# Performance work log

Measured on AMD Instinct MI355X. Metric: run time of the kernel, lower is better.

The kernel has to match this reference:

```python
import jax, jax.numpy as jnp
import numpy as np


def setup_inputs() -> dict:
    key = jax.random.key(0)
    ks = jax.random.split(key, 10)
    B, S, C, H, NC, T = 128, 512, 512, 512, 64, 25
    s = 0.02  # init scale
    return {
        "x": jax.random.normal(ks[0], (B, S, C), jnp.float32),
        "text": jax.random.randint(ks[1], (B, T + 1), 0, NC),
        "W_i2h": jax.random.normal(ks[2], (C, H), jnp.float32) * s,
        "W_h2h": jax.random.normal(ks[3], (H, H), jnp.float32) * s,
        "b_h2h": jnp.zeros((H,), jnp.float32),
        "W_score": jax.random.normal(ks[4], (H, 1), jnp.float32) * s,
        "W_lstm": jax.random.normal(ks[5], (C + NC, 4 * H), jnp.float32) * s,
        "U_lstm": jax.random.normal(ks[6], (H, 4 * H), jnp.float32) * s,
        "b_lstm": jnp.zeros((4 * H,), jnp.float32),
        "W_gen": jax.random.normal(ks[7], (H, NC), jnp.float32) * s,
        "b_gen": jnp.zeros((NC,), jnp.float32),
        "batch_max_length": 25,
    }


def reference(x, text, W_i2h, W_h2h, b_h2h, W_score, W_lstm, U_lstm, b_lstm,
              W_gen, b_gen, batch_max_length):
    B = x.shape[0]
    H = W_h2h.shape[0]
    NC = W_gen.shape[1]
    T = batch_max_length

    # i2h(batch_H) is loop-invariant -> compute once. [B,S,H]
    batch_H_proj = jnp.einsum('bsc,ch->bsh', x, W_i2h)
    # one-hot teacher-forcing inputs, time-major for scan. [T,B,NC]
    onehots_t = jnp.swapaxes(jax.nn.one_hot(text[:, :T], NC, dtype=x.dtype), 0, 1)

    def step(carry, char_oh):
        h, c = carry
        hp = (h @ W_h2h + b_h2h)[:, None, :]                 # [B,1,H]
        e = jnp.tanh(batch_H_proj + hp) @ W_score            # [B,S,1]
        alpha = jax.nn.softmax(e, axis=1)                    # [B,S,1]
        context = jnp.einsum('bs,bsc->bc', alpha[..., 0], x) # [B,C]
        inp = jnp.concatenate([context, char_oh], axis=1)    # [B,C+NC]
        # Keras LSTMCell gate math: z split into i,f,g,o chunks
        z = inp @ W_lstm + h @ U_lstm + b_lstm               # [B,4H]
        zi, zf, zg, zo = jnp.split(z, 4, axis=1)
        i = jax.nn.sigmoid(zi)
        f = jax.nn.sigmoid(zf)
        g = jnp.tanh(zg)
        o = jax.nn.sigmoid(zo)
        c_new = f * c + i * g
        h_new = o * jnp.tanh(c_new)
        return (h_new, c_new), h_new

    init = (jnp.zeros((B, H), x.dtype), jnp.zeros((B, H), x.dtype))
    _, hs = jax.lax.scan(step, init, onehots_t)              # [T,B,H]
    output_hiddens = jnp.swapaxes(hs, 0, 1)                  # [B,T,H]
    probs = output_hiddens @ W_gen + b_gen                   # [B,T,NC]
    return probs
```

## Files before the change

### kernel.cpp

```cpp
#include <hip/hip_runtime.h>
#include <hip/hip_bf16.h>

#define B_ 128
#define S_ 512
#define C_ 512
#define H_ 512
#define NC_ 64
#define T_ 25
#define TEXTW (T_ + 1)

typedef __attribute__((ext_vector_type(8))) short bf16x8;
typedef __attribute__((ext_vector_type(8))) unsigned short u16x8;
typedef __attribute__((ext_vector_type(4))) float f32x4;

__device__ __forceinline__ float bf2f(unsigned short u) {
    union { unsigned int i; float f; } v; v.i = ((unsigned int)u) << 16; return v.f;
}
__device__ __forceinline__ unsigned short f2bf(float f) {
    union { float f; unsigned int u; } v; v.f = f;
    unsigned int r = (v.u + 0x7FFFu + ((v.u >> 16) & 1u)) >> 16;
    return (unsigned short)r;
}
__device__ __forceinline__ void gload_lds16(const void* g, void* l) {
    __builtin_amdgcn_global_load_lds(
        (const __attribute__((address_space(1))) unsigned int*)g,
        (__attribute__((address_space(3))) unsigned int*)l, 16, 0, 0);
}
__device__ __forceinline__ float fast_tanh(float x) {
    float e = __builtin_amdgcn_exp2f(2.885390082f * x);
    return 1.f - 2.f * __builtin_amdgcn_rcpf(e + 1.f);
}
__device__ __forceinline__ float fast_sigmoid(float x) {
    return __builtin_amdgcn_rcpf(1.f + __builtin_amdgcn_exp2f(-1.442695041f * x));
}

__global__ __launch_bounds__(512) void setup_k(
    const float* __restrict__ Wi, const float* __restrict__ Wh,
    const float* __restrict__ Wl, const float* __restrict__ Ul,
    const float* __restrict__ bh,
    unsigned short* __restrict__ Wt_bf, unsigned short* __restrict__ Wh_bf,
    unsigned short* __restrict__ WU_t,
    float* __restrict__ c, float* __restrict__ hp, unsigned short* __restrict__ inp) {
    int blk = blockIdx.x, tid = threadIdx.x;
    if (blk < 128) {
        c[blk * 512 + tid] = 0.f;
        hp[blk * 512 + tid] = bh[tid];
        inp[blk * 1024 + 512 + tid] = 0;
    } else if (blk < 640) {
        int n = blk - 128;
        Wt_bf[n * 512 + tid] = f2bf(Wi[tid * 512 + n]);
    } else if (blk < 1152) {
        int i = (blk - 640) * 512 + tid;
        Wh_bf[i] = f2bf(Wh[i]);
    } else {
        int np = blk - 1152;
        int h = np >> 2, g = np & 3;
        {
            float v = Wl[(size_t)tid * 2048 + g * 512 + h];
            WU_t[(size_t)np * 1024 + tid] = f2bf(v);
        }
        {
            float v = Ul[(size_t)tid * 2048 + g * 512 + h];
            WU_t[(size_t)np * 1024 + 512 + tid] = f2bf(v);
        }
    }
}

__global__ __launch_bounds__(256) void conv_x(const float* __restrict__ in,
                                              unsigned short* __restrict__ out) {
    int i = blockIdx.x * 256 + threadIdx.x;
    const float4 v = ((const float4*)in)[i];
    ushort4 o;
    o.x = f2bf(v.x); o.y = f2bf(v.y); o.z = f2bf(v.z); o.w = f2bf(v.w);
    ((ushort4*)out)[i] = o;
}

__global__ __launch_bounds__(256) void gemm_proj(const unsigned short* __restrict__ A,
                                                 const unsigned short* __restrict__ Bt,
                                                 unsigned short* __restrict__ Cm) {
    __shared__ unsigned short As[128 * 64];
    __shared__ unsigned short Bs[128 * 64];
    int tid = threadIdx.x;
    int lane = tid & 63;
    int wid = tid >> 6;
    int wr = wid >> 1, wc = wid & 1;
    int row0 = blockIdx.y * 128;
    int col0 = blockIdx.x * 128;

    f32x4 acc[4][4];
#pragma unroll
    for (int i = 0; i < 4; ++i)
#pragma unroll
        for (int j = 0; j < 4; ++j) acc[i][j] = (f32x4){0.f, 0.f, 0.f, 0.f};

    for (int k0 = 0; k0 < 512; k0 += 64) {
#pragma unroll
        for (int i = 0; i < 4; ++i) {
            int e = tid + i * 256;
            int r = e >> 3, cc = e & 7;
            int cs = cc ^ (r & 7);
            gload_lds16(A + (size_t)(row0 + r) * 512 + k0 + cs * 8, &As[e * 8]);
        }
#pragma unroll
        for (int i = 0; i < 4; ++i) {
            int e = tid + i * 256;
            int r = e >> 3, cc = e & 7;
            int cs = cc ^ (r & 7);
            gload_lds16(Bt + (size_t)(col0 + r) * 512 + k0 + cs * 8, &Bs[e * 8]);
        }
        __syncthreads();
#pragma unroll
        for (int ks = 0; ks < 2; ++ks) {
            bf16x8 a[4], b[4];
#pragma unroll
            for (int i = 0; i < 4; ++i) {
                int m = wr * 64 + i * 16 + (lane & 15);
                int ch = (ks * 4 + (lane >> 4)) ^ (m & 7);
                a[i] = *(const bf16x8*)&As[(m * 8 + ch) * 8];
            }
#pragma unroll
            for (int j = 0; j < 4; ++j) {
                int n = wc * 64 + j * 16 + (lane & 15);
                int ch = (ks * 4 + (lane >> 4)) ^ (n & 7);
                b[j] = *(const bf16x8*)&Bs[(n * 8 + ch) * 8];
            }
#pragma unroll
            for (int i = 0; i < 4; ++i)
#pragma unroll
                for (int j = 0; j < 4; ++j)
                    acc[i][j] = __builtin_amdgcn_mfma_f32_16x16x32_bf16(a[i], b[j], acc[i][j], 0, 0, 0);
        }
        __syncthreads();
    }
#pragma unroll
    for (int i = 0; i < 4; ++i)
#pragma unroll
        for (int j = 0; j < 4; ++j) {
            int gcol = col0 + wc * 64 + j * 16 + (lane & 15);
#pragma unroll
            for (int r = 0; r < 4; ++r) {
                int grow = row0 + wr * 64 + i * 16 + (lane >> 4) * 4 + r;
                Cm[(size_t)grow * 512 + gcol] = f2bf(acc[i][j][r]);
            }
        }
}

__global__ __launch_bounds__(1024) void ectx_kernel(
    const unsigned short* __restrict__ proj, const unsigned short* __restrict__ xb,
    const float* __restrict__ hp, const float* __restrict__ Wscore,
    unsigned short* __restrict__ inp) {
    __shared__ float sh_e[512];
    __shared__ float sh_alpha[512];
    __shared__ float sh_red[16];
    __shared__ float shp[8][512];
    int b = blockIdx.x;
    int tid = threadIdx.x, wave = tid >> 6, lane = tid & 63;

    {
        float4 h0 = *(const float4*)(hp + b * 512 + lane * 8);
        float4 h1 = *(const float4*)(hp + b * 512 + lane * 8 + 4);
        float4 w0 = *(const float4*)(Wscore + lane * 8);
        float4 w1 = *(const float4*)(Wscore + lane * 8 + 4);
        float hp_r[8] = {h0.x, h0.y, h0.z, h0.w, h1.x, h1.y, h1.z, h1.w};
        float w_r[8]  = {w0.x, w0.y, w0.z, w0.w, w1.x, w1.y, w1.z, w1.w};
        float w2_r[8];
#pragma unroll
        for (int j = 0; j < 8; ++j) w2_r[j] = -2.f * w_r[j];
        int s0 = wave * 32;
        for (int i = 0; i < 32; i += 4) {
            bf16x8 pv[4];
#pragma unroll
            for (int q = 0; q < 4; ++q)
                pv[q] = *(const bf16x8*)(proj + ((size_t)(b * 512 + s0 + i + q) << 9) + lane * 8);
#pragma unroll
            for (int q = 0; q < 4; ++q) {
                float a = 0.f;
#pragma unroll
                for (int j = 0; j < 8; ++j) {
                    float xv = bf2f((unsigned short)pv[q][j]) + hp_r[j];
                    float r = __builtin_amdgcn_rcpf(__builtin_amdgcn_exp2f(2.885390082f * xv) + 1.f);
                    a += w_r[j];
                    a = fmaf(w2_r[j], r, a);
                }
#pragma unroll
                for (int off = 32; off > 0; off >>= 1) a += __shfl_xor(a, off, 64);
                if (lane == 0) sh_e[s0 + i + q] = a;
            }
        }
    }
    __syncthreads();

    if (tid < 512) {
        float v = sh_e[tid];
        float m = v;
#pragma unroll
        for (int off = 32; off > 0; off >>= 1) m = fmaxf(m, __shfl_xor(m, off, 64));
        if (lane == 0) sh_red[wave] = m;
    }
    __syncthreads();
    if (tid < 512) {
        float v = sh_e[tid];
        float mm = sh_red[0];
#pragma unroll
        for (int i = 1; i < 8; ++i) mm = fmaxf(mm, sh_red[i]);
        float p = __builtin_amdgcn_exp2f(1.442695041f * (v - mm));
        float ss = p;
#pragma unroll
        for (int off = 32; off > 0; off >>= 1) ss += __shfl_xor(ss, off, 64);
        if (lane == 0) sh_red[8 + wave] = ss;
        sh_alpha[tid] = p;
    }
    __syncthreads();
    {
        float tot = 0.f;
#pragma unroll
        for (int i = 0; i < 8; ++i) tot += sh_red[8 + i];
        float inv = __builtin_amdgcn_rcpf(tot);
        inv = inv * (2.f - tot * inv);
        if (tid < 512) sh_alpha[tid] = sh_alpha[tid] * inv;
    }
    __syncthreads();

    {
        int cc = wave >> 3, sg = wave & 7;
        int col = cc * 256 + lane * 4;
        float a0 = 0.f, a1 = 0.f, a2 = 0.f, a3 = 0.f;
#pragma unroll 4
        for (int s = sg; s < 512; s += 8) {
            float al = sh_alpha[s];
            ushort4 xv = *(const ushort4*)(xb + ((size_t)(b * 512 + s) << 9) + col);
            a0 = fmaf(al, bf2f(xv.x), a0);
            a1 = fmaf(al, bf2f(xv.y), a1);
            a2 = fmaf(al, bf2f(xv.z), a2);
            a3 = fmaf(al, bf2f(xv.w), a3);
        }
        *(float4*)&shp[sg][col] = make_float4(a0, a1, a2, a3);
    }
    __syncthreads();
    if (tid < 512) {
        float s = 0.f;
#pragma unroll
        for (int r = 0; r < 8; ++r) s += shp[r][tid];
        inp[b * 1024 + tid] = f2bf(s);
    }
}

__global__ __launch_bounds__(512) void z_gemm(const unsigned short* __restrict__ A,
                                              const unsigned short* __restrict__ Bt,
                                              float* __restrict__ Z) {
    __shared__ unsigned short As[8192];
    __shared__ unsigned short Bs[4096];
    int tid = threadIdx.x;
    int lane = tid & 63;
    int wave = tid >> 6;
    int wr = wave >> 2, wc = wave & 3;
    int col0 = blockIdx.x * 64;

    f32x4 acc[4];
#pragma unroll
    for (int i = 0; i < 4; ++i) acc[i] = (f32x4){0.f, 0.f, 0.f, 0.f};

    for (int k0 = 0; k0 < 1024; k0 += 64) {
#pragma unroll
        for (int i = 0; i < 2; ++i) {
            int e = tid + i * 512;
            int r = e >> 3, cc = e & 7;
            int cs = cc ^ (r & 7);
            gload_lds16(A + (size_t)r * 1024 + k0 + cs * 8, &As[e * 8]);
        }
        {
            int e = tid;
            int r = e >> 3, cc = e & 7;
            int cs = cc ^ (r & 7);
            gload_lds16(Bt + (size_t)(col0 + r) * 1024 + k0 + cs * 8, &Bs[e * 8]);
        }
        __syncthreads();
#pragma unroll
        for (int ks = 0; ks < 2; ++ks) {
            bf16x8 a[4], bfr;
#pragma unroll
            for (int i = 0; i < 4; ++i) {
                int m = wr * 64 + i * 16 + (lane & 15);
                int ch = (ks * 4 + (lane >> 4)) ^ (m & 7);
                a[i] = *(const bf16x8*)&As[(m * 8 + ch) * 8];
            }
            {
                int n = wc * 16 + (lane & 15);
                int ch = (ks * 4 + (lane >> 4)) ^ (n & 7);
                bfr = *(const bf16x8*)&Bs[(n * 8 + ch) * 8];
            }
#pragma unroll
            for (int i = 0; i < 4; ++i)
                acc[i] = __builtin_amdgcn_mfma_f32_16x16x32_bf16(a[i], bfr, acc[i], 0, 0, 0);
        }
        __syncthreads();
    }
#pragma unroll
    for (int i = 0; i < 4; ++i) {
        int gcol = col0 + wc * 16 + (lane & 15);
#pragma unroll
        for (int r = 0; r < 4; ++r) {
            int grow = wr * 64 + i * 16 + (lane >> 4) * 4 + r;
            Z[(size_t)grow * 2048 + gcol] = acc[i][r];
        }
    }
}

__global__ __launch_bounds__(512) void ghp_kernel(
    const float* __restrict__ z, const int* __restrict__ text,
    const float* __restrict__ Wl, const float* __restrict__ bl,
    const unsigned short* __restrict__ Whb, const float* __restrict__ bh2h,
    float* __restrict__ c, float* __restrict__ hs_t,
    unsigned short* __restrict__ inp, float* __restrict__ hp_buf, int t) {
    __shared__ float shg[512];
    __shared__ float gp[8][512];
    int b = blockIdx.x, tid = threadIdx.x;
    int wave = tid >> 6, lane = tid & 63;
    int ch = text[b * TEXTW + t];
    const float* wrow = Wl + (size_t)(512 + ch) * 2048;
    float4 zv = *(const float4*)(z + (size_t)b * 2048 + tid * 4);
    float zi = zv.x + bl[tid] + wrow[tid];
    float zf = zv.y + bl[512 + tid] + wrow[512 + tid];
    float zg = zv.z + bl[1024 + tid] + wrow[1024 + tid];
    float zo = zv.w + bl[1536 + tid] + wrow[1536 + tid];
    float ig = fast_sigmoid(zi);
    float fg = fast_sigmoid(zf);
    float gg = fast_tanh(zg);
    float og = fast_sigmoid(zo);
    int idx = b * 512 + tid;
    float cn = fg * c[idx] + ig * gg;
    c[idx] = cn;
    float hn = og * fast_tanh(cn);
    hs_t[idx] = hn;
    inp[b * 1024 + 512 + tid] = f2bf(hn);
    shg[tid] = hn;
    __syncthreads();
    float r8[8] = {0.f, 0.f, 0.f, 0.f, 0.f, 0.f, 0.f, 0.f};
    for (int kk = 0; kk < 64; ++kk) {
        int k = wave * 64 + kk;
        float hv = shg[k];
        u16x8 wv = *(const u16x8*)(Whb + k * 512 + lane * 8);
#pragma unroll
        for (int jj = 0; jj < 8; ++jj) r8[jj] = fmaf(hv, bf2f(wv[jj]), r8[jj]);
    }
#pragma unroll
    for (int jj = 0; jj < 8; ++jj) gp[wave][lane * 8 + jj] = r8[jj];
    __syncthreads();
    float s = bh2h[tid];
#pragma unroll
    for (int w = 0; w < 8; ++w) s += gp[w][tid];
    hp_buf[b * 512 + tid] = s;
}

__global__ __launch_bounds__(64) void gen_probs(const float* __restrict__ hs,
                                                const float* __restrict__ Wg,
                                                const float* __restrict__ bg,
                                                float* __restrict__ out) {
    __shared__ float sh[512];
    int bt = blockIdx.x;
    int b = bt / T_, t = bt % T_;
    int tid = threadIdx.x;
    const float* hrow = hs + ((size_t)t * B_ + b) * H_;
    for (int i = tid; i < 512; i += 64) sh[i] = hrow[i];
    __syncthreads();
    float acc = bg[tid];
#pragma unroll 4
    for (int k = 0; k < 512; ++k) acc = fmaf(sh[k], Wg[k * 64 + tid], acc);
    out[(size_t)bt * 64 + tid] = acc;
}

extern "C" void kernel_launch(void* const* d_in, const int* in_sizes, int n_in,
                              void* d_out, int out_size, void* d_ws, size_t ws_size,
                              hipStream_t stream) {
    const float* x       = (const float*)d_in[0];
    const int*   text    = (const int*)d_in[1];
    const float* W_i2h   = (const float*)d_in[2];
    const float* W_h2h   = (const float*)d_in[3];
    const float* b_h2h   = (const float*)d_in[4];
    const float* W_score = (const float*)d_in[5];
    const float* W_lstm  = (const float*)d_in[6];
    const float* U_lstm  = (const float*)d_in[7];
    const float* b_lstm  = (const float*)d_in[8];
    const float* W_gen   = (const float*)d_in[9];
    const float* b_gen   = (const float*)d_in[10];
    float* out = (float*)d_out;

    char* ws = (char*)d_ws;
    unsigned short* x_bf    = (unsigned short*)ws;
    unsigned short* proj_bf = (unsigned short*)(ws + 67108864);
    unsigned short* Wt_bf   = (unsigned short*)(ws + 134217728);
    unsigned short* Wh_bf   = (unsigned short*)(ws + 134742016);
    unsigned short* WU_t    = (unsigned short*)(ws + 135266304);
    float* c_buf   = (float*)(ws + 139460608);
    float* hp_buf  = (float*)(ws + 139722752);
    unsigned short* inp_bf = (unsigned short*)(ws + 140247040);
    float* z_buf   = (float*)(ws + 140509184);
    float* hs      = (float*)(ws + 141557760);

    setup_k<<<dim3(3200), 512, 0, stream>>>(W_i2h, W_h2h, W_lstm, U_lstm, b_h2h,
                                            Wt_bf, Wh_bf, WU_t, c_buf, hp_buf, inp_bf);
    conv_x<<<dim3(32768), 256, 0, stream>>>(x, x_bf);
    gemm_proj<<<dim3(4, 512), 256, 0, stream>>>(x_bf, Wt_bf, proj_bf);
    for (int t = 0; t < T_; ++t) {
        ectx_kernel<<<dim3(128), 1024, 0, stream>>>(proj_bf, x_bf, hp_buf, W_score, inp_bf);
        z_gemm<<<dim3(32), 512, 0, stream>>>(inp_bf, WU_t, z_buf);
        ghp_kernel<<<dim3(128), 512, 0, stream>>>(z_buf, text, W_lstm, b_lstm,
                                                  Wh_bf, b_h2h, c_buf,
                                                  hs + (size_t)t * (B_ * H_),
                                                  inp_bf, hp_buf, t);
    }
    gen_probs<<<dim3(B_ * T_), 64, 0, stream>>>(hs, W_gen, b_gen, out);
}
```

Before: 1.552 ms.

## Fuse LSTM gate/h2h step with next step's attention context kernel

Merges the per-step gate/h2h kernel with the following attention-context kernel into one 1024-thread kernel. The h2h projection now stays in shared memory instead of going through a global hp buffer, and its K loop is split across 16 waves instead of 8. The first step runs a special t=-1 launch that seeds the projection with the bias, and the last step returns early so it skips the unused h2h and attention work. This drops one launch per timestep and a global round trip, at the cost of more shared memory and the gate phase running on only half the threads.

```diff
diff --git a/kernel.cpp b/kernel.cpp
--- a/kernel.cpp
+++ b/kernel.cpp
@@ -37,14 +37,12 @@
 __global__ __launch_bounds__(512) void setup_k(
     const float* __restrict__ Wi, const float* __restrict__ Wh,
     const float* __restrict__ Wl, const float* __restrict__ Ul,
-    const float* __restrict__ bh,
     unsigned short* __restrict__ Wt_bf, unsigned short* __restrict__ Wh_bf,
     unsigned short* __restrict__ WU_t,
-    float* __restrict__ c, float* __restrict__ hp, unsigned short* __restrict__ inp) {
+    float* __restrict__ c, unsigned short* __restrict__ inp) {
     int blk = blockIdx.x, tid = threadIdx.x;
     if (blk < 128) {
         c[blk * 512 + tid] = 0.f;
-        hp[blk * 512 + tid] = bh[tid];
         inp[blk * 1024 + 512 + tid] = 0;
     } else if (blk < 640) {
         int n = blk - 128;
@@ -145,10 +143,78 @@
         }
 }
 
-__global__ __launch_bounds__(1024) void ectx_kernel(
+__global__ __launch_bounds__(512) void z_gemm(const unsigned short* __restrict__ A,
+                                              const unsigned short* __restrict__ Bt,
+                                              float* __restrict__ Z) {
+    __shared__ unsigned short As[8192];
+    __shared__ unsigned short Bs[4096];
+    int tid = threadIdx.x;
+    int lane = tid & 63;
+    int wave = tid >> 6;
+    int wr = wave >> 2, wc = wave & 3;
+    int col0 = blockIdx.x * 64;
+
+    f32x4 acc[4];
+#pragma unroll
+    for (int i = 0; i < 4; ++i) acc[i] = (f32x4){0.f, 0.f, 0.f, 0.f};
+
+    for (int k0 = 0; k0 < 1024; k0 += 64) {
+#pragma unroll
+        for (int i = 0; i < 2; ++i) {
+            int e = tid + i * 512;
+            int r = e >> 3, cc = e & 7;
+            int cs = cc ^ (r & 7);
+            gload_lds16(A + (size_t)r * 1024 + k0 + cs * 8, &As[e * 8]);
+        }
+        {
+            int e = tid;
+            int r = e >> 3, cc = e & 7;
+            int cs = cc ^ (r & 7);
+            gload_lds16(Bt + (size_t)(col0 + r) * 1024 + k0 + cs * 8, &Bs[e * 8]);
+        }
+        __syncthreads();
+#pragma unroll
+        for (int ks = 0; ks < 2; ++ks) {
+            bf16x8 a[4], bfr;
+#pragma unroll
+            for (int i = 0; i < 4; ++i) {
+                int m = wr * 64 + i * 16 + (lane & 15);
+                int ch = (ks * 4 + (lane >> 4)) ^ (m & 7);
+                a[i] = *(const bf16x8*)&As[(m * 8 + ch) * 8];
+            }
+            {
+                int n = wc * 16 + (lane & 15);
+                int ch = (ks * 4 + (lane >> 4)) ^ (n & 7);
+                bfr = *(const bf16x8*)&Bs[(n * 8 + ch) * 8];
+            }
+#pragma unroll
+            for (int i = 0; i < 4; ++i)
+                acc[i] = __builtin_amdgcn_mfma_f32_16x16x32_bf16(a[i], bfr, acc[i], 0, 0, 0);
+        }
+        __syncthreads();
+    }
+#pragma unroll
+    for (int i = 0; i < 4; ++i) {
+        int gcol = col0 + wc * 16 + (lane & 15);
+#pragma unroll
+        for (int r = 0; r < 4; ++r) {
+            int grow = wr * 64 + i * 16 + (lane >> 4) * 4 + r;
+            Z[(size_t)grow * 2048 + gcol] = acc[i][r];
+        }
+    }
+}
+
+__global__ __launch_bounds__(1024) void ghp_ectx(
+    const float* __restrict__ z, const int* __restrict__ text,
+    const float* __restrict__ Wl, const float* __restrict__ bl,
+    const unsigned short* __restrict__ Whb, const float* __restrict__ bh2h,
+    float* __restrict__ c, float* __restrict__ hs_t,
+    unsigned short* __restrict__ inp,
     const unsigned short* __restrict__ proj, const unsigned short* __restrict__ xb,
-    const float* __restrict__ hp, const float* __restrict__ Wscore,
-    unsigned short* __restrict__ inp) {
+    const float* __restrict__ Wscore, int t) {
+    __shared__ float shg[512];
+    __shared__ float gp[16][512];
+    __shared__ float sh_hp[512];
     __shared__ float sh_e[512];
     __shared__ float sh_alpha[512];
     __shared__ float sh_red[16];
@@ -156,9 +222,58 @@
     int b = blockIdx.x;
     int tid = threadIdx.x, wave = tid >> 6, lane = tid & 63;
 
+    if (t >= 0) {
+        if (tid < 512) {
+            int ch = text[b * TEXTW + t];
+            const float* wrow = Wl + (size_t)(512 + ch) * 2048;
+            float4 zv = *(const float4*)(z + (size_t)b * 2048 + tid * 4);
+            float zi = zv.x + bl[tid] + wrow[tid];
+            float zf = zv.y + bl[512 + tid] + wrow[512 + tid];
+            float zg = zv.z + bl[1024 + tid] + wrow[1024 + tid];
+            float zo = zv.w + bl[1536 + tid] + wrow[1536 + tid];
+            float ig = fast_sigmoid(zi);
+            float fg = fast_sigmoid(zf);
+            float gg = fast_tanh(zg);
+            float og = fast_sigmoid(zo);
+            int idx = b * 512 + tid;
+            float cn = fg * c[idx] + ig * gg;
+            c[idx] = cn;
+            float hn = og * fast_tanh(cn);
+            hs_t[idx] = hn;
+            inp[b * 1024 + 512 + tid] = f2bf(hn);
+            shg[tid] = hn;
+        }
+        __syncthreads();
+        if (t >= T_ - 1) return;
+        {
+            float r8[8] = {0.f, 0.f, 0.f, 0.f, 0.f, 0.f, 0.f, 0.f};
+#pragma unroll 4
+            for (int kk = 0; kk < 32; ++kk) {
+                int k = wave * 32 + kk;
+                float hv = shg[k];
+                u16x8 wv = *(const u16x8*)(Whb + k * 512 + lane * 8);
+#pragma unroll
+                for (int jj = 0; jj < 8; ++jj) r8[jj] = fmaf(hv, bf2f(wv[jj]), r8[jj]);
+            }
+#pragma unroll
+            for (int jj = 0; jj < 8; ++jj) gp[wave][lane * 8 + jj] = r8[jj];
+        }
+        __syncthreads();
+        if (tid < 512) {
+            float s = bh2h[tid];
+#pragma unroll
+            for (int w = 0; w < 16; ++w) s += gp[w][tid];
+            sh_hp[tid] = s;
+        }
+        __syncthreads();
+    } else {
+        if (tid < 512) sh_hp[tid] = bh2h[tid];
+        __syncthreads();
+    }
+
     {
-        float4 h0 = *(const float4*)(hp + b * 512 + lane * 8);
-        float4 h1 = *(const float4*)(hp + b * 512 + lane * 8 + 4);
+        float4 h0 = *(const float4*)(sh_hp + lane * 8);
+        float4 h1 = *(const float4*)(sh_hp + lane * 8 + 4);
         float4 w0 = *(const float4*)(Wscore + lane * 8);
         float4 w1 = *(const float4*)(Wscore + lane * 8 + 4);
         float hp_r[8] = {h0.x, h0.y, h0.z, h0.w, h1.x, h1.y, h1.z, h1.w};
@@ -243,113 +358,6 @@
         for (int r = 0; r < 8; ++r) s += shp[r][tid];
         inp[b * 1024 + tid] = f2bf(s);
     }
-}
-
-__global__ __launch_bounds__(512) void z_gemm(const unsigned short* __restrict__ A,
-                                              const unsigned short* __restrict__ Bt,
-                                              float* __restrict__ Z) {
-    __shared__ unsigned short As[8192];
-    __shared__ unsigned short Bs[4096];
-    int tid = threadIdx.x;
-    int lane = tid & 63;
-    int wave = tid >> 6;
-    int wr = wave >> 2, wc = wave & 3;
-    int col0 = blockIdx.x * 64;
-
-    f32x4 acc[4];
-#pragma unroll
-    for (int i = 0; i < 4; ++i) acc[i] = (f32x4){0.f, 0.f, 0.f, 0.f};
-
-    for (int k0 = 0; k0 < 1024; k0 += 64) {
-#pragma unroll
-        for (int i = 0; i < 2; ++i) {
-            int e = tid + i * 512;
-            int r = e >> 3, cc = e & 7;
-            int cs = cc ^ (r & 7);
-            gload_lds16(A + (size_t)r * 1024 + k0 + cs * 8, &As[e * 8]);
-        }
-        {
-            int e = tid;
-            int r = e >> 3, cc = e & 7;
-            int cs = cc ^ (r & 7);
-            gload_lds16(Bt + (size_t)(col0 + r) * 1024 + k0 + cs * 8, &Bs[e * 8]);
-        }
-        __syncthreads();
-#pragma unroll
-        for (int ks = 0; ks < 2; ++ks) {
-            bf16x8 a[4], bfr;
-#pragma unroll
-            for (int i = 0; i < 4; ++i) {
-                int m = wr * 64 + i * 16 + (lane & 15);
-                int ch = (ks * 4 + (lane >> 4)) ^ (m & 7);
-                a[i] = *(const bf16x8*)&As[(m * 8 + ch) * 8];
-            }
-            {
-                int n = wc * 16 + (lane & 15);
-                int ch = (ks * 4 + (lane >> 4)) ^ (n & 7);
-                bfr = *(const bf16x8*)&Bs[(n * 8 + ch) * 8];
-            }
-#pragma unroll
-            for (int i = 0; i < 4; ++i)
-                acc[i] = __builtin_amdgcn_mfma_f32_16x16x32_bf16(a[i], bfr, acc[i], 0, 0, 0);
-        }
-        __syncthreads();
-    }
-#pragma unroll
-    for (int i = 0; i < 4; ++i) {
-        int gcol = col0 + wc * 16 + (lane & 15);
-#pragma unroll
-        for (int r = 0; r < 4; ++r) {
-            int grow = wr * 64 + i * 16 + (lane >> 4) * 4 + r;
-            Z[(size_t)grow * 2048 + gcol] = acc[i][r];
-        }
-    }
-}
-
-__global__ __launch_bounds__(512) void ghp_kernel(
-    const float* __restrict__ z, const int* __restrict__ text,
-    const float* __restrict__ Wl, const float* __restrict__ bl,
-    const unsigned short* __restrict__ Whb, const float* __restrict__ bh2h,
-    float* __restrict__ c, float* __restrict__ hs_t,
-    unsigned short* __restrict__ inp, float* __restrict__ hp_buf, int t) {
-    __shared__ float shg[512];
-    __shared__ float gp[8][512];
-    int b = blockIdx.x, tid = threadIdx.x;
-    int wave = tid >> 6, lane = tid & 63;
-    int ch = text[b * TEXTW + t];
-    const float* wrow = Wl + (size_t)(512 + ch) * 2048;
-    float4 zv = *(const float4*)(z + (size_t)b * 2048 + tid * 4);
-    float zi = zv.x + bl[tid] + wrow[tid];
-    float zf = zv.y + bl[512 + tid] + wrow[512 + tid];
-    float zg = zv.z + bl[1024 + tid] + wrow[1024 + tid];
-    float zo = zv.w + bl[1536 + tid] + wrow[1536 + tid];
-    float ig = fast_sigmoid(zi);
-    float fg = fast_sigmoid(zf);
-    float gg = fast_tanh(zg);
-    float og = fast_sigmoid(zo);
-    int idx = b * 512 + tid;
-    float cn = fg * c[idx] + ig * gg;
-    c[idx] = cn;
-    float hn = og * fast_tanh(cn);
-    hs_t[idx] = hn;
-    inp[b * 1024 + 512 + tid] = f2bf(hn);
-    shg[tid] = hn;
-    __syncthreads();
-    float r8[8] = {0.f, 0.f, 0.f, 0.f, 0.f, 0.f, 0.f, 0.f};
-    for (int kk = 0; kk < 64; ++kk) {
-        int k = wave * 64 + kk;
-        float hv = shg[k];
-        u16x8 wv = *(const u16x8*)(Whb + k * 512 + lane * 8);
-#pragma unroll
-        for (int jj = 0; jj < 8; ++jj) r8[jj] = fmaf(hv, bf2f(wv[jj]), r8[jj]);
-    }
-#pragma unroll
-    for (int jj = 0; jj < 8; ++jj) gp[wave][lane * 8 + jj] = r8[jj];
-    __syncthreads();
-    float s = bh2h[tid];
-#pragma unroll
-    for (int w = 0; w < 8; ++w) s += gp[w][tid];
-    hp_buf[b * 512 + tid] = s;
 }
 
 __global__ __launch_bounds__(64) void gen_probs(const float* __restrict__ hs,
@@ -392,22 +400,21 @@
     unsigned short* Wh_bf   = (unsigned short*)(ws + 134742016);
     unsigned short* WU_t    = (unsigned short*)(ws + 135266304);
     float* c_buf   = (float*)(ws + 139460608);
-    float* hp_buf  = (float*)(ws + 139722752);
     unsigned short* inp_bf = (unsigned short*)(ws + 140247040);
     float* z_buf   = (float*)(ws + 140509184);
     float* hs      = (float*)(ws + 141557760);
 
-    setup_k<<<dim3(3200), 512, 0, stream>>>(W_i2h, W_h2h, W_lstm, U_lstm, b_h2h,
-                                            Wt_bf, Wh_bf, WU_t, c_buf, hp_buf, inp_bf);
+    setup_k<<<dim3(3200), 512, 0, stream>>>(W_i2h, W_h2h, W_lstm, U_lstm,
+                                            Wt_bf, Wh_bf, WU_t, c_buf, inp_bf);
     conv_x<<<dim3(32768), 256, 0, stream>>>(x, x_bf);
     gemm_proj<<<dim3(4, 512), 256, 0, stream>>>(x_bf, Wt_bf, proj_bf);
+    ghp_ectx<<<dim3(128), 1024, 0, stream>>>(z_buf, text, W_lstm, b_lstm, Wh_bf, b_h2h,
+                                             c_buf, hs, inp_bf, proj_bf, x_bf, W_score, -1);
     for (int t = 0; t < T_; ++t) {
-        ectx_kernel<<<dim3(128), 1024, 0, stream>>>(proj_bf, x_bf, hp_buf, W_score, inp_bf);
         z_gemm<<<dim3(32), 512, 0, stream>>>(inp_bf, WU_t, z_buf);
-        ghp_kernel<<<dim3(128), 512, 0, stream>>>(z_buf, text, W_lstm, b_lstm,
-                                                  Wh_bf, b_h2h, c_buf,
-                                                  hs + (size_t)t * (B_ * H_),
-                                                  inp_bf, hp_buf, t);
+        ghp_ectx<<<dim3(128), 1024, 0, stream>>>(z_buf, text, W_lstm, b_lstm, Wh_bf, b_h2h,
+                                                 c_buf, hs + (size_t)t * (B_ * H_),
+                                                 inp_bf, proj_bf, x_bf, W_score, t);
     }
     gen_probs<<<dim3(B_ * T_), 64, 0, stream>>>(hs, W_gen, b_gen, out);
 }
```

Result: faster. 1.494 ms (-3.7%).
